# Performance work log

Measured on AMD Instinct MI355X. Metric: run time of the kernel, lower is better.

Reference implementation:

```python
import jax, jax.numpy as jnp
import numpy as np

NH = 8
MIN_LOG, MAX_LOG, P_SCALE = -12.0, 0.0, 1.0
EPS = 1e-6


def setup_inputs() -> dict:
    key = jax.random.key(0)
    ks = jax.random.split(key, 8)
    B, H, W, C = 2, 512, 64, 256
    s = lambda k, shape, sc: jax.random.normal(k, shape, jnp.float32) * sc
    return {
        "x": jax.random.normal(ks[0], (B, H, W, C), jnp.float32),
        "pos": jax.random.uniform(ks[1], (B, H, 4), dtype=jnp.float32),
        "Wq": s(ks[2], (C, 2 * C), 0.02),
        "Wk": s(ks[3], (C, C), 0.02),
        "Wv": s(ks[4], (C, C), 0.02),
        "Wo": s(ks[5], (C, C), 0.02),
        "bo": jnp.zeros((C,), jnp.float32),
        "q_norm_w": jnp.ones((C // NH,), jnp.float32),
        "k_norm_w": jnp.ones((C // NH,), jnp.float32),
        "rope_w": s(ks[6], (4,), 0.5),
        "rope_b": jnp.zeros((1,), jnp.float32),
    }


def _rmsnorm(x, w):
    # QWEN3-style RMSNorm in fp32, per-head last dim
    xf = x.astype(jnp.float32)
    var = jnp.mean(xf * xf, axis=-1, keepdims=True)
    return (w * xf * jax.lax.rsqrt(var + EPS)).astype(x.dtype)


def reference(x, pos, Wq, Wk, Wv, Wo, bo, q_norm_w, k_norm_w, rope_w, rope_b):
    B, H, W, C = x.shape
    nh = NH
    hd = C // nh          # head_dim (= rope_dim, even)
    half = hd // 2
    # [B,H,W,C] -> [B*W, H, C]: attention along trace axis H per time w
    xr = jnp.transpose(x, (0, 2, 1, 3)).reshape(B * W, H, C)
    qg = xr @ Wq                                  # [BW,H,2C]
    q, gate = qg[..., :C], qg[..., C:]            # elementwise output gate
    q = q.reshape(B * W, H, nh, hd).transpose(0, 2, 1, 3)   # [BW,nh,H,hd]
    k = (xr @ Wk).reshape(B * W, H, nh, hd).transpose(0, 2, 1, 3)
    v = (xr @ Wv).reshape(B * W, H, nh, hd).transpose(0, 2, 1, 3)
    q = _rmsnorm(q, q_norm_w)
    k = _rmsnorm(k, k_norm_w)
    # segmented-exponential RoPE: linear mapper pos -> scalar p, log-spaced freqs
    p = pos @ rope_w + rope_b[0]                  # [B,H]
    freqs = jnp.exp(jnp.linspace(MIN_LOG, MAX_LOG, nh * half, dtype=jnp.float32))
    ang = (p[..., None] * P_SCALE) * freqs        # [B,H,nh*half]
    ang = ang.reshape(B, H, nh, half).transpose(0, 2, 1, 3)   # [B,nh,H,half]
    cos = jnp.cos(ang)[:, None]                   # [B,1,nh,H,half]
    sin = jnp.sin(ang)[:, None]

    def rot(t):  # t: [B,W,nh,H,hd], interleaved (even,odd) pairs
        t = t.reshape(B, W, nh, H, half, 2)
        e, o = t[..., 0], t[..., 1]
        e2 = e * cos - o * sin
        o2 = e * sin + o * cos
        return jnp.stack([e2, o2], axis=-1).reshape(B * W, nh, H, hd)

    q = rot(q.reshape(B, W, nh, H, hd))
    k = rot(k.reshape(B, W, nh, H, hd))
    scale = hd ** (-0.5)
    attn = jax.nn.softmax(jnp.einsum('bnqd,bnkd->bnqk', q, k) * scale, axis=-1)
    out = jnp.einsum('bnqk,bnkd->bnqd', attn, v).transpose(0, 2, 1, 3)  # [BW,H,nh,hd]
    out = out * jax.nn.sigmoid(gate.reshape(B * W, H, nh, hd))
    out = out.reshape(B * W, H, C) @ Wo + bo
    out = out.reshape(B, W, H, C)
    return jnp.transpose(out, (0, 2, 1, 3))       # [B,H,W,C]
```

## Files before the change

kernel.cpp:

```cpp
#include <hip/hip_runtime.h>
#include <hip/hip_bf16.h>
#include <math.h>

#define NHEADS 8
#define HDIM   32
#define HALFD  16
#define DB     2
#define DH     512
#define DW     64
#define DC     256
#define NTOK   (DB*DW*DH)

typedef unsigned short u16;
typedef unsigned int   u32;
typedef short short8 __attribute__((ext_vector_type(8)));
typedef float f32x4  __attribute__((ext_vector_type(4)));

__device__ __forceinline__ float bf_lo(u32 u){ union{u32 i; float f;} c; c.i = u << 16; return c.f; }
__device__ __forceinline__ float bf_hi(u32 u){ union{u32 i; float f;} c; c.i = u & 0xffff0000u; return c.f; }
__device__ __forceinline__ float bfu(u16 u){ union{u32 i; float f;} c; c.i = ((u32)u) << 16; return c.f; }
__device__ __forceinline__ u16 f2bf(float f){
    u32 x = __float_as_uint(f);
    u32 r = (x + 0x7fffu + ((x >> 16) & 1u)) >> 16;
    return (u16)r;
}
__device__ __forceinline__ u16 f2bf_fast(float f){
    return (u16)((__float_as_uint(f) + 0x8000u) >> 16);
}
__device__ __forceinline__ u32 cvtpk(float a, float b){
    u32 r; asm("v_cvt_pk_bf16_f32 %0, %1, %2" : "=v"(r) : "v"(a), "v"(b)); return r;
}
__device__ __forceinline__ void gload_lds16(const u16* g, u16* l){
    __builtin_amdgcn_global_load_lds(
        (const __attribute__((address_space(1))) void*)g,
        (__attribute__((address_space(3))) void*)l, 16, 0, 0);
}

__global__ void __launch_bounds__(256) prep_kernel(
    const float* __restrict__ pos, const float* __restrict__ rope_w,
    const float* __restrict__ rope_b, float* __restrict__ cosT, float* __restrict__ sinT,
    const float* __restrict__ Wq, const float* __restrict__ Wk,
    const float* __restrict__ Wv, const float* __restrict__ Wo,
    u16* __restrict__ Wfl, u16* __restrict__ Wofl)
{
    int bid = blockIdx.x;
    if (bid < 512) {
        int id = bid * 256 + threadIdx.x;
        int j = id & 15;
        int n = (id >> 4) & 7;
        int h = (id >> 7) & 511;
        int b = id >> 16;
        const float* pp = pos + (size_t)(b*DH + h)*4;
        float p = pp[0]*rope_w[0] + pp[1]*rope_w[1] + pp[2]*rope_w[2] + pp[3]*rope_w[3] + rope_b[0];
        int fi = n*HALFD + j;
        float freq = expf(-12.0f + (float)fi * (12.0f/127.0f));
        float ang = p * freq;
        cosT[id] = cosf(ang);
        sinT[id] = sinf(ang);
    } else {
        int eid = (bid - 512)*256 + threadIdx.x;
        if (eid < 32768) {
            int nn = eid >> 5, k0 = (eid & 31)*8;
            const float* src; int ld, nl;
            if (nn < 512)      { src = Wq; ld = 512; nl = nn;       }
            else if (nn < 768) { src = Wk; ld = 256; nl = nn - 512; }
            else               { src = Wv; ld = 256; nl = nn - 768; }
            union { short8 s; uint4 u; } c;
            #pragma unroll
            for (int j = 0; j < 8; ++j) c.s[j] = (short)f2bf(src[(size_t)(k0+j)*ld + nl]);
            int ct = nn >> 7, r2 = nn & 127;
            int cs = r2 >> 6, nf = (r2 >> 4) & 3, lq = r2 & 15;
            int ks = k0 >> 5, g = (k0 >> 3) & 3;
            size_t off = (size_t)ct*32768 + (ks*8 + cs*4 + nf)*512 + (g*16 + lq)*8;
            *reinterpret_cast<uint4*>(Wfl + off) = c.u;
        } else {
            int e2 = eid - 32768;
            int nn = e2 >> 5, k0 = (e2 & 31)*8;
            union { short8 s; uint4 u; } c;
            #pragma unroll
            for (int j = 0; j < 8; ++j) c.s[j] = (short)f2bf(Wo[(size_t)(k0+j)*256 + nn]);
            int ct = nn >> 7, r2 = nn & 127;
            int cs = r2 >> 6, nf = (r2 >> 4) & 3, lq = r2 & 15;
            int ks = k0 >> 5, g = (k0 >> 3) & 3;
            size_t off = (size_t)ct*32768 + (ks*8 + cs*4 + nf)*512 + (g*16 + lq)*8;
            *reinterpret_cast<uint4*>(Wofl + off) = c.u;
        }
    }
}

__global__ void __launch_bounds__(256, 1) proj_mfma_kernel(
    const float* __restrict__ x, const u16* __restrict__ Wfl, u16* __restrict__ QGKV)
{
    __shared__ u16 BUF[2][32768];
    int tid = threadIdx.x;
    int rt  = blockIdx.x;
    int lane = tid & 63, wv = tid >> 6;
    int g = lane >> 4, lq = lane & 15;
    int rhalf = wv >> 1, cstrip = wv & 1;

    #pragma unroll
    for (int r = 0; r < 16; ++r)
        gload_lds16(Wfl + (r*256 + tid)*8, &BUF[0][(r*256 + tid)*8]);
    __builtin_amdgcn_sched_barrier(0);

    {
        int i  = tid >> 1;
        int kg = tid & 1;
        int t  = rt*128 + i;
        int bw = t >> 9, h = t & 511, b = bw >> 6, w = bw & 63;
        const float* xr = x + ((size_t)((b*DH + h)*DW + w))*DC;
        int rb = i >> 4, r = i & 15;
        #pragma unroll
        for (int kk = 0; kk < 16; ++kk) {
            int k0 = kg*128 + kk*8;
            float4 f0 = *reinterpret_cast<const float4*>(xr + k0);
            float4 f1 = *reinterpret_cast<const float4*>(xr + k0 + 4);
            uint4 c;
            c.x = cvtpk(f0.x, f0.y); c.y = cvtpk(f0.z, f0.w);
            c.z = cvtpk(f1.x, f1.y); c.w = cvtpk(f1.z, f1.w);
            int ks = k0 >> 5, gg = (k0 >> 3) & 3;
            *reinterpret_cast<uint4*>(&BUF[1][(ks*8+rb)*512 + (gg*16+r)*8]) = c;
        }
    }
    __syncthreads();

    short8 xf[4][8];
    #pragma unroll
    for (int tf = 0; tf < 4; ++tf)
        #pragma unroll
        for (int ks = 0; ks < 8; ++ks) {
            union { uint4 u; short8 s; } c;
            c.u = *reinterpret_cast<const uint4*>(&BUF[1][(ks*8 + rhalf*4 + tf)*512 + lane*8]);
            xf[tf][ks] = c.s;
        }
    asm volatile("s_waitcnt lgkmcnt(0)" ::: "memory");
    __builtin_amdgcn_sched_barrier(0);
    asm volatile("s_waitcnt vmcnt(0)" ::: "memory");
    __syncthreads();

    for (int ct = 0; ct < 8; ++ct) {
        u16* cur = BUF[ct & 1];
        u16* nxt = BUF[(ct & 1) ^ 1];
        if (ct + 1 < 8) {
            const u16* src = Wfl + (size_t)(ct + 1)*32768;
            #pragma unroll
            for (int r = 0; r < 16; ++r)
                gload_lds16(src + (r*256 + tid)*8, &nxt[(r*256 + tid)*8]);
        }
        __builtin_amdgcn_sched_barrier(0);

        int nbase = ct*128 + cstrip*64;
        f32x4 acc[4][4];
        #pragma unroll
        for (int a = 0; a < 4; ++a)
            #pragma unroll
            for (int bb = 0; bb < 4; ++bb) acc[a][bb] = (f32x4){0.f,0.f,0.f,0.f};

        #pragma unroll
        for (int ks = 0; ks < 8; ++ks) {
            short8 wf[4];
            #pragma unroll
            for (int nf = 0; nf < 4; ++nf) {
                union { uint4 u; short8 s; } c;
                c.u = *reinterpret_cast<const uint4*>(&cur[(ks*8 + cstrip*4 + nf)*512 + lane*8]);
                wf[nf] = c.s;
            }
            #pragma unroll
            for (int tf = 0; tf < 4; ++tf)
                #pragma unroll
                for (int nf = 0; nf < 4; ++nf)
                    acc[tf][nf] = __builtin_amdgcn_mfma_f32_16x16x32_bf16(wf[nf], xf[tf][ks], acc[tf][nf], 0, 0, 0);
        }
        #pragma unroll
        for (int tf = 0; tf < 4; ++tf) {
            int trow = rt*128 + (rhalf*4 + tf)*16 + lq;
            u16* dst = QGKV + (size_t)trow*1024 + nbase;
            #pragma unroll
            for (int nf = 0; nf < 4; ++nf) {
                uint2 w2;
                w2.x = cvtpk(acc[tf][nf][0], acc[tf][nf][1]);
                w2.y = cvtpk(acc[tf][nf][2], acc[tf][nf][3]);
                *reinterpret_cast<uint2*>(dst + nf*16 + g*4) = w2;
            }
        }
        asm volatile("s_waitcnt vmcnt(0)" ::: "memory");
        __syncthreads();
    }
}

__global__ void __launch_bounds__(512) attn_kernel(
    u16* __restrict__ QGKV,
    const float* __restrict__ qnw, const float* __restrict__ knw,
    const float* __restrict__ cosT, const float* __restrict__ sinT)
{
    __shared__ u16 KL[512*32];
    __shared__ u16 VL[2*8192];
    __shared__ u16 QP[512*32];

    int bid  = blockIdx.x;
    int bw   = bid >> 3, n = bid & 7;
    int tid  = threadIdx.x;
    int lane = tid & 63;
    int wv   = tid >> 6;
    int g    = lane >> 4;
    int lq   = lane & 15;
    const float CSC = 0.17677669529663687f * 1.4426950408889634f;

    {
        int i = tid;
        size_t tb = ((size_t)(bw*DH + i))*1024;
        int b = bw >> 6;
        int tbl = ((b*DH + i)*NHEADS + n)*HALFD;
        float cs[16], sn[16];
        #pragma unroll
        for (int j4 = 0; j4 < 4; ++j4) {
            float4 c4 = *reinterpret_cast<const float4*>(cosT + tbl + j4*4);
            float4 s4 = *reinterpret_cast<const float4*>(sinT + tbl + j4*4);
            cs[j4*4+0]=c4.x; cs[j4*4+1]=c4.y; cs[j4*4+2]=c4.z; cs[j4*4+3]=c4.w;
            sn[j4*4+0]=s4.x; sn[j4*4+1]=s4.y; sn[j4*4+2]=s4.z; sn[j4*4+3]=s4.w;
        }
        int rb = i >> 4, r = i & 15;
        #pragma unroll
        for (int which = 0; which < 2; ++which) {
            const u16* srcp = QGKV + tb + (which ? 512 : 0) + n*HDIM;
            const float* nw = which ? knw : qnw;
            u16* dstL = which ? KL : QP;
            uint4 rr[4];
            #pragma unroll
            for (int ii = 0; ii < 4; ++ii) rr[ii] = reinterpret_cast<const uint4*>(srcp)[ii];
            float v[32]; float ss = 0.f;
            const u32* rw = reinterpret_cast<const u32*>(rr);
            #pragma unroll
            for (int ii = 0; ii < 16; ++ii) {
                v[2*ii]   = bf_lo(rw[ii]);
                v[2*ii+1] = bf_hi(rw[ii]);
                ss += v[2*ii]*v[2*ii] + v[2*ii+1]*v[2*ii+1];
            }
            float rs = rsqrtf(ss*(1.0f/32.0f) + 1e-6f);
            if (which == 0) rs *= CSC;
            #pragma unroll
            for (int d = 0; d < 32; ++d) v[d] *= rs * nw[d];
            #pragma unroll
            for (int j = 0; j < 16; ++j) {
                float e = v[2*j], o = v[2*j+1];
                v[2*j]   = e*cs[j] - o*sn[j];
                v[2*j+1] = e*sn[j] + o*cs[j];
            }
            #pragma unroll
            for (int gg = 0; gg < 4; ++gg) {
                uint4 u;
                u.x = (u32)f2bf(v[8*gg+0]) | ((u32)f2bf(v[8*gg+1]) << 16);
                u.y = (u32)f2bf(v[8*gg+2]) | ((u32)f2bf(v[8*gg+3]) << 16);
                u.z = (u32)f2bf(v[8*gg+4]) | ((u32)f2bf(v[8*gg+5]) << 16);
                u.w = (u32)f2bf(v[8*gg+6]) | ((u32)f2bf(v[8*gg+7]) << 16);
                *reinterpret_cast<uint4*>(dstL + rb*512 + gg*128 + r*8) = u;
            }
        }
        const uint4* vsrc = reinterpret_cast<const uint4*>(QGKV + tb + 768 + n*HDIM);
        uint4 v0 = vsrc[0], v1 = vsrc[1], v2 = vsrc[2], v3 = vsrc[3];
        *reinterpret_cast<uint4*>(VL + i*16)          = v0;
        *reinterpret_cast<uint4*>(VL + i*16 + 8)      = v1;
        *reinterpret_cast<uint4*>(VL + 8192 + i*16)   = v2;
        *reinterpret_cast<uint4*>(VL + 8192 + i*16+8) = v3;
    }
    __syncthreads();

    short8 qf[4];
    #pragma unroll
    for (int qt = 0; qt < 4; ++qt) {
        union { uint4 u; short8 s; } c;
        c.u = *reinterpret_cast<const uint4*>(QP + (wv*4 + qt)*512 + lane*8);
        qf[qt] = c.s;
    }

    f32x4 oacc[4][2];
    float l_run[4];
    #pragma unroll
    for (int qt = 0; qt < 4; ++qt) {
        oacc[qt][0] = (f32x4){0.f,0.f,0.f,0.f};
        oacc[qt][1] = (f32x4){0.f,0.f,0.f,0.f};
        l_run[qt] = 0.f;
    }

    u16* PW = QP + wv*2048;
    const int sw = (lq ^ (lq >> 2)) & 3;
    const u32 vbase = (u32)(uintptr_t)VL + (u32)(lq*8 + g*256);

    for (int st = 0; st < 16; ++st) {
        short8 kf[2];
        #pragma unroll
        for (int kt = 0; kt < 2; ++kt) {
            union { uint4 u; short8 s; } c;
            c.u = *reinterpret_cast<const uint4*>(KL + (st*2 + kt)*512 + lane*8);
            kf[kt] = c.s;
        }
        uint2 v00, v01, v10, v11;
        {
            u32 ta = vbase + (u32)(st*1024);
            asm volatile("ds_read_b64_tr_b16 %0, %4\n\t"
                         "ds_read_b64_tr_b16 %1, %4 offset:128\n\t"
                         "ds_read_b64_tr_b16 %2, %4 offset:16384\n\t"
                         "ds_read_b64_tr_b16 %3, %4 offset:16512"
                         : "=v"(v00), "=v"(v01), "=v"(v10), "=v"(v11)
                         : "v"(ta));
        }
        #pragma unroll
        for (int qt = 0; qt < 4; ++qt) {
            __builtin_amdgcn_s_setprio(1);
            f32x4 sf0 = __builtin_amdgcn_mfma_f32_16x16x32_bf16(kf[0], qf[qt], (f32x4){0.f,0.f,0.f,0.f}, 0, 0, 0);
            f32x4 sf1 = __builtin_amdgcn_mfma_f32_16x16x32_bf16(kf[1], qf[qt], (f32x4){0.f,0.f,0.f,0.f}, 0, 0, 0);
            __builtin_amdgcn_s_setprio(0);
            float p0 = __builtin_amdgcn_exp2f(sf0[0]);
            float p1 = __builtin_amdgcn_exp2f(sf0[1]);
            float p2 = __builtin_amdgcn_exp2f(sf0[2]);
            float p3 = __builtin_amdgcn_exp2f(sf0[3]);
            float p4 = __builtin_amdgcn_exp2f(sf1[0]);
            float p5 = __builtin_amdgcn_exp2f(sf1[1]);
            float p6 = __builtin_amdgcn_exp2f(sf1[2]);
            float p7 = __builtin_amdgcn_exp2f(sf1[3]);
            l_run[qt] += ((p0+p1)+(p2+p3)) + ((p4+p5)+(p6+p7));
            int row = qt*16 + lq;
            int ch0 = ((g >> 1)    ) ^ sw;
            int ch1 = ((g >> 1) + 2) ^ sw;
            uint2 w0, w1;
            w0.x = cvtpk(p0, p1); w0.y = cvtpk(p2, p3);
            w1.x = cvtpk(p4, p5); w1.y = cvtpk(p6, p7);
            *reinterpret_cast<uint2*>(PW + row*32 + ch0*8 + (g&1)*4) = w0;
            *reinterpret_cast<uint2*>(PW + row*32 + ch1*8 + (g&1)*4) = w1;
        }
        short8 pb[4];
        #pragma unroll
        for (int qt = 0; qt < 4; ++qt) {
            int row = qt*16 + lq;
            union { uint4 u; short8 s; } c;
            c.u = *reinterpret_cast<const uint4*>(PW + row*32 + (g ^ sw)*8);
            pb[qt] = c.s;
        }
        asm volatile("s_waitcnt lgkmcnt(0)" ::: "memory");
        __builtin_amdgcn_sched_barrier(0);
        union { uint4 u; short8 s; } va0, va1;
        va0.u = make_uint4(v00.x, v00.y, v01.x, v01.y);
        va1.u = make_uint4(v10.x, v10.y, v11.x, v11.y);
        __builtin_amdgcn_s_setprio(1);
        #pragma unroll
        for (int qt = 0; qt < 4; ++qt) {
            oacc[qt][0] = __builtin_amdgcn_mfma_f32_16x16x32_bf16(va0.s, pb[qt], oacc[qt][0], 0, 0, 0);
            oacc[qt][1] = __builtin_amdgcn_mfma_f32_16x16x32_bf16(va1.s, pb[qt], oacc[qt][1], 0, 0, 0);
        }
        __builtin_amdgcn_s_setprio(0);
    }

    #pragma unroll
    for (int qt = 0; qt < 4; ++qt) {
        float lr = l_run[qt];
        lr += __shfl_xor(lr, 16);
        lr += __shfl_xor(lr, 32);
        float inv = 1.0f / lr;
        int t = bw*DH + wv*64 + qt*16 + lq;
        size_t tb = (size_t)t*1024;
        #pragma unroll
        for (int df = 0; df < 2; ++df) {
            int col = n*HDIM + 16*df + 4*g;
            ushort4 gv = *reinterpret_cast<const ushort4*>(QGKV + tb + 256 + col);
            u16 gr[4] = {gv.x, gv.y, gv.z, gv.w};
            ushort4 ov;
            u16 orr[4];
            #pragma unroll
            for (int r = 0; r < 4; ++r) {
                float o  = oacc[qt][df][r] * inv;
                float gf = bfu(gr[r]);
                float sg = 1.0f / (1.0f + __builtin_amdgcn_exp2f(-gf * 1.4426950408889634f));
                orr[r] = f2bf_fast(o * sg);
            }
            ov.x = orr[0]; ov.y = orr[1]; ov.z = orr[2]; ov.w = orr[3];
            *reinterpret_cast<ushort4*>(QGKV + tb + col) = ov;
        }
    }
}

__global__ void __launch_bounds__(256, 1) outproj_mfma_kernel(
    const u16* __restrict__ QGKV, const u16* __restrict__ Wofl,
    const float* __restrict__ bo, float* __restrict__ out)
{
    __shared__ u16 BUF[2][32768];
    int tid = threadIdx.x;
    int rt  = blockIdx.x;
    int lane = tid & 63, wv = tid >> 6;
    int g = lane >> 4, lq = lane & 15;
    int rhalf = wv >> 1, cstrip = wv & 1;

    #pragma unroll
    for (int r = 0; r < 16; ++r)
        gload_lds16(Wofl + (r*256 + tid)*8, &BUF[0][(r*256 + tid)*8]);
    __builtin_amdgcn_sched_barrier(0);

    {
        int i  = tid >> 1;
        int kg = tid & 1;
        const u16* arow = QGKV + (size_t)(rt*128 + i)*1024;
        int rb = i >> 4, r = i & 15;
        #pragma unroll
        for (int kk = 0; kk < 16; ++kk) {
            int k0 = kg*128 + kk*8;
            uint4 u = *reinterpret_cast<const uint4*>(arow + k0);
            int ks = k0 >> 5, gg = (k0 >> 3) & 3;
            *reinterpret_cast<uint4*>(&BUF[1][(ks*8+rb)*512 + (gg*16+r)*8]) = u;
        }
    }
    __syncthreads();

    short8 xf[4][8];
    #pragma unroll
    for (int tf = 0; tf < 4; ++tf)
        #pragma unroll
        for (int ks = 0; ks < 8; ++ks) {
            union { uint4 u; short8 s; } c;
            c.u = *reinterpret_cast<const uint4*>(&BUF[1][(ks*8 + rhalf*4 + tf)*512 + lane*8]);
            xf[tf][ks] = c.s;
        }
    asm volatile("s_waitcnt lgkmcnt(0)" ::: "memory");
    __builtin_amdgcn_sched_barrier(0);
    asm volatile("s_waitcnt vmcnt(0)" ::: "memory");
    __syncthreads();

    for (int ct = 0; ct < 2; ++ct) {
        u16* cur = BUF[ct & 1];
        u16* nxt = BUF[(ct & 1) ^ 1];
        if (ct + 1 < 2) {
            const u16* src = Wofl + (size_t)(ct + 1)*32768;
            #pragma unroll
            for (int r = 0; r < 16; ++r)
                gload_lds16(src + (r*256 + tid)*8, &nxt[(r*256 + tid)*8]);
        }
        __builtin_amdgcn_sched_barrier(0);

        int nbase = ct*128 + cstrip*64;
        f32x4 acc[4][4];
        #pragma unroll
        for (int a = 0; a < 4; ++a)
            #pragma unroll
            for (int bb = 0; bb < 4; ++bb) acc[a][bb] = (f32x4){0.f,0.f,0.f,0.f};

        #pragma unroll
        for (int ks = 0; ks < 8; ++ks) {
            short8 wf[4];
            #pragma unroll
            for (int nf = 0; nf < 4; ++nf) {
                union { uint4 u; short8 s; } c;
                c.u = *reinterpret_cast<const uint4*>(&cur[(ks*8 + cstrip*4 + nf)*512 + lane*8]);
                wf[nf] = c.s;
            }
            #pragma unroll
            for (int tf = 0; tf < 4; ++tf)
                #pragma unroll
                for (int nf = 0; nf < 4; ++nf)
                    acc[tf][nf] = __builtin_amdgcn_mfma_f32_16x16x32_bf16(wf[nf], xf[tf][ks], acc[tf][nf], 0, 0, 0);
        }
        #pragma unroll
        for (int tf = 0; tf < 4; ++tf) {
            int trow = rt*128 + (rhalf*4 + tf)*16 + lq;
            int bw = trow >> 9, h = trow & 511, b = bw >> 6, w = bw & 63;
            float* orow = out + ((size_t)((b*DH + h)*DW + w))*DC;
            #pragma unroll
            for (int nf = 0; nf < 4; ++nf) {
                int nn = nbase + nf*16 + g*4;
                float4 bv = *reinterpret_cast<const float4*>(bo + nn);
                float4 res;
                res.x = acc[tf][nf][0] + bv.x;
                res.y = acc[tf][nf][1] + bv.y;
                res.z = acc[tf][nf][2] + bv.z;
                res.w = acc[tf][nf][3] + bv.w;
                *reinterpret_cast<float4*>(orow + nn) = res;
            }
        }
        asm volatile("s_waitcnt vmcnt(0)" ::: "memory");
        __syncthreads();
    }
}

extern "C" void kernel_launch(void* const* d_in, const int* in_sizes, int n_in,
                              void* d_out, int out_size, void* d_ws, size_t ws_size,
                              hipStream_t stream)
{
    const float* x      = (const float*)d_in[0];
    const float* pos    = (const float*)d_in[1];
    const float* Wq     = (const float*)d_in[2];
    const float* Wk     = (const float*)d_in[3];
    const float* Wv     = (const float*)d_in[4];
    const float* Wo     = (const float*)d_in[5];
    const float* bo     = (const float*)d_in[6];
    const float* qnw    = (const float*)d_in[7];
    const float* knw    = (const float*)d_in[8];
    const float* rope_w = (const float*)d_in[9];
    const float* rope_b = (const float*)d_in[10];
    float* out = (float*)d_out;

    char* wsp = (char*)d_ws;
    u16*   QGKV = (u16*)wsp;
    float* cosT = (float*)(wsp + (size_t)NTOK*1024*2);
    float* sinT = cosT + DB*DH*NHEADS*HALFD;
    u16*   Wfl  = (u16*)(sinT + DB*DH*NHEADS*HALFD);
    u16*   Wofl = Wfl + 8*32768;

    prep_kernel        <<<dim3(672),  dim3(256), 0, stream>>>(pos, rope_w, rope_b, cosT, sinT,
                                                              Wq, Wk, Wv, Wo, Wfl, Wofl);
    proj_mfma_kernel   <<<dim3(512),  dim3(256), 0, stream>>>(x, Wfl, QGKV);
    attn_kernel        <<<dim3(1024), dim3(512), 0, stream>>>(QGKV, qnw, knw, cosT, sinT);
    outproj_mfma_kernel<<<dim3(512),  dim3(256), 0, stream>>>(QGKV, Wofl, bo, out);
}
```

Baseline: 208.4 us.

## Compute Q in registers, shrink P scratch, interleave PV MFMA, remap block order

Q normalization and RoPE are now computed directly into MFMA fragments in registers, with cross-lane shuffles for the RMS sum, so the Q staging buffer in shared memory is no longer needed. The P scratch shrinks to a double-buffered 16-row slab per wave, and each PV MFMA is issued right after its own P tile is written instead of after all four tiles. Shared memory drops enough that launch_bounds can request more resident blocks. Block indices are also permuted so that consecutive blocks share the same head. The risks are extra LDS dependency stalls from the per-tile write/read round trip and register pressure under the tighter launch bound.

```diff
diff --git a/kernel.cpp b/kernel.cpp
--- a/kernel.cpp
+++ b/kernel.cpp
@@ -188,28 +188,29 @@
     }
 }
 
-__global__ void __launch_bounds__(512) attn_kernel(
+__global__ void __launch_bounds__(512, 4) attn_kernel(
     u16* __restrict__ QGKV,
     const float* __restrict__ qnw, const float* __restrict__ knw,
     const float* __restrict__ cosT, const float* __restrict__ sinT)
 {
     __shared__ u16 KL[512*32];
     __shared__ u16 VL[2*8192];
-    __shared__ u16 QP[512*32];
-
-    int bid  = blockIdx.x;
-    int bw   = bid >> 3, n = bid & 7;
+    __shared__ u16 PL[8192];
+
+    int bid0 = blockIdx.x;
+    int idx  = (bid0 & 7)*128 + (bid0 >> 3);
+    int bw   = idx >> 3, n = idx & 7;
     int tid  = threadIdx.x;
     int lane = tid & 63;
     int wv   = tid >> 6;
     int g    = lane >> 4;
     int lq   = lane & 15;
+    int b    = bw >> 6;
     const float CSC = 0.17677669529663687f * 1.4426950408889634f;
 
     {
         int i = tid;
         size_t tb = ((size_t)(bw*DH + i))*1024;
-        int b = bw >> 6;
         int tbl = ((b*DH + i)*NHEADS + n)*HALFD;
         float cs[16], sn[16];
         #pragma unroll
@@ -219,42 +220,36 @@
             cs[j4*4+0]=c4.x; cs[j4*4+1]=c4.y; cs[j4*4+2]=c4.z; cs[j4*4+3]=c4.w;
             sn[j4*4+0]=s4.x; sn[j4*4+1]=s4.y; sn[j4*4+2]=s4.z; sn[j4*4+3]=s4.w;
         }
+        const u16* srcp = QGKV + tb + 512 + n*HDIM;
+        uint4 rr[4];
+        #pragma unroll
+        for (int ii = 0; ii < 4; ++ii) rr[ii] = reinterpret_cast<const uint4*>(srcp)[ii];
+        float v[32]; float ss = 0.f;
+        const u32* rw = reinterpret_cast<const u32*>(rr);
+        #pragma unroll
+        for (int ii = 0; ii < 16; ++ii) {
+            v[2*ii]   = bf_lo(rw[ii]);
+            v[2*ii+1] = bf_hi(rw[ii]);
+            ss += v[2*ii]*v[2*ii] + v[2*ii+1]*v[2*ii+1];
+        }
+        float rs = rsqrtf(ss*(1.0f/32.0f) + 1e-6f);
+        #pragma unroll
+        for (int d = 0; d < 32; ++d) v[d] *= rs * knw[d];
+        #pragma unroll
+        for (int j = 0; j < 16; ++j) {
+            float e = v[2*j], o = v[2*j+1];
+            v[2*j]   = e*cs[j] - o*sn[j];
+            v[2*j+1] = e*sn[j] + o*cs[j];
+        }
         int rb = i >> 4, r = i & 15;
         #pragma unroll
-        for (int which = 0; which < 2; ++which) {
-            const u16* srcp = QGKV + tb + (which ? 512 : 0) + n*HDIM;
-            const float* nw = which ? knw : qnw;
-            u16* dstL = which ? KL : QP;
-            uint4 rr[4];
-            #pragma unroll
-            for (int ii = 0; ii < 4; ++ii) rr[ii] = reinterpret_cast<const uint4*>(srcp)[ii];
-            float v[32]; float ss = 0.f;
-            const u32* rw = reinterpret_cast<const u32*>(rr);
-            #pragma unroll
-            for (int ii = 0; ii < 16; ++ii) {
-                v[2*ii]   = bf_lo(rw[ii]);
-                v[2*ii+1] = bf_hi(rw[ii]);
-                ss += v[2*ii]*v[2*ii] + v[2*ii+1]*v[2*ii+1];
-            }
-            float rs = rsqrtf(ss*(1.0f/32.0f) + 1e-6f);
-            if (which == 0) rs *= CSC;
-            #pragma unroll
-            for (int d = 0; d < 32; ++d) v[d] *= rs * nw[d];
-            #pragma unroll
-            for (int j = 0; j < 16; ++j) {
-                float e = v[2*j], o = v[2*j+1];
-                v[2*j]   = e*cs[j] - o*sn[j];
-                v[2*j+1] = e*sn[j] + o*cs[j];
-            }
-            #pragma unroll
-            for (int gg = 0; gg < 4; ++gg) {
-                uint4 u;
-                u.x = (u32)f2bf(v[8*gg+0]) | ((u32)f2bf(v[8*gg+1]) << 16);
-                u.y = (u32)f2bf(v[8*gg+2]) | ((u32)f2bf(v[8*gg+3]) << 16);
-                u.z = (u32)f2bf(v[8*gg+4]) | ((u32)f2bf(v[8*gg+5]) << 16);
-                u.w = (u32)f2bf(v[8*gg+6]) | ((u32)f2bf(v[8*gg+7]) << 16);
-                *reinterpret_cast<uint4*>(dstL + rb*512 + gg*128 + r*8) = u;
-            }
+        for (int gg = 0; gg < 4; ++gg) {
+            uint4 u;
+            u.x = (u32)f2bf(v[8*gg+0]) | ((u32)f2bf(v[8*gg+1]) << 16);
+            u.y = (u32)f2bf(v[8*gg+2]) | ((u32)f2bf(v[8*gg+3]) << 16);
+            u.z = (u32)f2bf(v[8*gg+4]) | ((u32)f2bf(v[8*gg+5]) << 16);
+            u.w = (u32)f2bf(v[8*gg+6]) | ((u32)f2bf(v[8*gg+7]) << 16);
+            *reinterpret_cast<uint4*>(KL + rb*512 + gg*128 + r*8) = u;
         }
         const uint4* vsrc = reinterpret_cast<const uint4*>(QGKV + tb + 768 + n*HDIM);
         uint4 v0 = vsrc[0], v1 = vsrc[1], v2 = vsrc[2], v3 = vsrc[3];
@@ -263,15 +258,48 @@
         *reinterpret_cast<uint4*>(VL + 8192 + i*16)   = v2;
         *reinterpret_cast<uint4*>(VL + 8192 + i*16+8) = v3;
     }
+
+    short8 qf[4];
+    {
+        float qw[8];
+        {
+            float4 a = *reinterpret_cast<const float4*>(qnw + g*8);
+            float4 c = *reinterpret_cast<const float4*>(qnw + g*8 + 4);
+            qw[0]=a.x; qw[1]=a.y; qw[2]=a.z; qw[3]=a.w;
+            qw[4]=c.x; qw[5]=c.y; qw[6]=c.z; qw[7]=c.w;
+        }
+        #pragma unroll
+        for (int qt = 0; qt < 4; ++qt) {
+            int hrow = wv*64 + qt*16 + lq;
+            union { uint4 u; u32 w[4]; } qr;
+            qr.u = *reinterpret_cast<const uint4*>(
+                QGKV + ((size_t)(bw*DH + hrow))*1024 + n*HDIM + g*8);
+            float v[8]; float ss = 0.f;
+            #pragma unroll
+            for (int ii = 0; ii < 4; ++ii) {
+                v[2*ii]   = bf_lo(qr.w[ii]);
+                v[2*ii+1] = bf_hi(qr.w[ii]);
+                ss += v[2*ii]*v[2*ii] + v[2*ii+1]*v[2*ii+1];
+            }
+            ss += __shfl_xor(ss, 16);
+            ss += __shfl_xor(ss, 32);
+            float rs = rsqrtf(ss*(1.0f/32.0f) + 1e-6f) * CSC;
+            int tbl = ((b*DH + hrow)*NHEADS + n)*HALFD + g*4;
+            float4 c4 = *reinterpret_cast<const float4*>(cosT + tbl);
+            float4 s4 = *reinterpret_cast<const float4*>(sinT + tbl);
+            float cs[4] = {c4.x, c4.y, c4.z, c4.w};
+            float sn[4] = {s4.x, s4.y, s4.z, s4.w};
+            union { short8 s8; u32 w[4]; } o;
+            #pragma unroll
+            for (int p = 0; p < 4; ++p) {
+                float e  = v[2*p]   * rs * qw[2*p];
+                float od = v[2*p+1] * rs * qw[2*p+1];
+                o.w[p] = cvtpk(e*cs[p] - od*sn[p], e*sn[p] + od*cs[p]);
+            }
+            qf[qt] = o.s8;
+        }
+    }
     __syncthreads();
-
-    short8 qf[4];
-    #pragma unroll
-    for (int qt = 0; qt < 4; ++qt) {
-        union { uint4 u; short8 s; } c;
-        c.u = *reinterpret_cast<const uint4*>(QP + (wv*4 + qt)*512 + lane*8);
-        qf[qt] = c.s;
-    }
 
     f32x4 oacc[4][2];
     float l_run[4];
@@ -282,7 +310,7 @@
         l_run[qt] = 0.f;
     }
 
-    u16* PW = QP + wv*2048;
+    u16* PW = PL + wv*1024;
     const int sw = (lq ^ (lq >> 2)) & 3;
     const u32 vbase = (u32)(uintptr_t)VL + (u32)(lq*8 + g*256);
 
@@ -304,6 +332,7 @@
                          : "=v"(v00), "=v"(v01), "=v"(v10), "=v"(v11)
                          : "v"(ta));
         }
+        union { uint4 u; short8 s; } va0, va1;
         #pragma unroll
         for (int qt = 0; qt < 4; ++qt) {
             __builtin_amdgcn_s_setprio(1);
@@ -319,35 +348,27 @@
             float p6 = __builtin_amdgcn_exp2f(sf1[2]);
             float p7 = __builtin_amdgcn_exp2f(sf1[3]);
             l_run[qt] += ((p0+p1)+(p2+p3)) + ((p4+p5)+(p6+p7));
-            int row = qt*16 + lq;
+            u16* pq = PW + (qt & 1)*512 + lq*32;
             int ch0 = ((g >> 1)    ) ^ sw;
             int ch1 = ((g >> 1) + 2) ^ sw;
             uint2 w0, w1;
             w0.x = cvtpk(p0, p1); w0.y = cvtpk(p2, p3);
             w1.x = cvtpk(p4, p5); w1.y = cvtpk(p6, p7);
-            *reinterpret_cast<uint2*>(PW + row*32 + ch0*8 + (g&1)*4) = w0;
-            *reinterpret_cast<uint2*>(PW + row*32 + ch1*8 + (g&1)*4) = w1;
-        }
-        short8 pb[4];
-        #pragma unroll
-        for (int qt = 0; qt < 4; ++qt) {
-            int row = qt*16 + lq;
-            union { uint4 u; short8 s; } c;
-            c.u = *reinterpret_cast<const uint4*>(PW + row*32 + (g ^ sw)*8);
-            pb[qt] = c.s;
-        }
-        asm volatile("s_waitcnt lgkmcnt(0)" ::: "memory");
-        __builtin_amdgcn_sched_barrier(0);
-        union { uint4 u; short8 s; } va0, va1;
-        va0.u = make_uint4(v00.x, v00.y, v01.x, v01.y);
-        va1.u = make_uint4(v10.x, v10.y, v11.x, v11.y);
-        __builtin_amdgcn_s_setprio(1);
-        #pragma unroll
-        for (int qt = 0; qt < 4; ++qt) {
-            oacc[qt][0] = __builtin_amdgcn_mfma_f32_16x16x32_bf16(va0.s, pb[qt], oacc[qt][0], 0, 0, 0);
-            oacc[qt][1] = __builtin_amdgcn_mfma_f32_16x16x32_bf16(va1.s, pb[qt], oacc[qt][1], 0, 0, 0);
-        }
-        __builtin_amdgcn_s_setprio(0);
+            *reinterpret_cast<uint2*>(pq + ch0*8 + (g&1)*4) = w0;
+            *reinterpret_cast<uint2*>(pq + ch1*8 + (g&1)*4) = w1;
+            union { uint4 u; short8 s; } pb;
+            pb.u = *reinterpret_cast<const uint4*>(pq + (g ^ sw)*8);
+            if (qt == 0) {
+                asm volatile("s_waitcnt lgkmcnt(0)" ::: "memory");
+                __builtin_amdgcn_sched_barrier(0);
+                va0.u = make_uint4(v00.x, v00.y, v01.x, v01.y);
+                va1.u = make_uint4(v10.x, v10.y, v11.x, v11.y);
+            }
+            __builtin_amdgcn_s_setprio(1);
+            oacc[qt][0] = __builtin_amdgcn_mfma_f32_16x16x32_bf16(va0.s, pb.s, oacc[qt][0], 0, 0, 0);
+            oacc[qt][1] = __builtin_amdgcn_mfma_f32_16x16x32_bf16(va1.s, pb.s, oacc[qt][1], 0, 0, 0);
+            __builtin_amdgcn_s_setprio(0);
+        }
     }
 
     #pragma unroll
```

Measured after the change: 180.5 us, median of 4. 1.15x faster.
